# Optimization experiments

Measured on AMD Instinct MI355X. Metric: run time of the kernel, lower is better.

Reference implementation:

```python
import math
import jax, jax.numpy as jnp
import numpy as np

D_MODEL = 1024
NHEAD = 16
NUM_TEMP = 4
HEAD = D_MODEL // NHEAD          # 64
DIM = HEAD // NUM_TEMP           # 16
SCALE = math.sqrt(HEAD)
B, L = 2, 2048


def _make_freq():
    # freq = 10000^(-arange(0,dim,2)/dim), repeat_interleave(2) -> length DIM
    f = np.power(10000.0, -np.arange(0, DIM, 2) / DIM)
    return jnp.asarray(np.repeat(f, 2), dtype=jnp.float32)  # (DIM,)


def setup_inputs() -> dict:
    key = jax.random.key(0)
    ks = jax.random.split(key, 8)
    s = 0.02
    return {
        "data": jax.random.normal(ks[0], (B, L, D_MODEL), jnp.float32),
        "temporal": jax.random.uniform(ks[1], (B, L, NUM_TEMP), jnp.float32),
        "mask": jnp.zeros((L, L), jnp.float32),
        "Wq": jax.random.normal(ks[2], (D_MODEL, D_MODEL), jnp.float32) * s,
        "bq": jnp.zeros((D_MODEL,), jnp.float32),
        "Wk": jax.random.normal(ks[3], (D_MODEL, D_MODEL), jnp.float32) * s,
        "bk": jnp.zeros((D_MODEL,), jnp.float32),
        "Wv": jax.random.normal(ks[4], (D_MODEL, D_MODEL), jnp.float32) * s,
        "bv": jnp.zeros((D_MODEL,), jnp.float32),
    }


def _rotate_half_pairs(x):
    # [-x2, x1, -x4, x3, ...] along last dim
    stacked = jnp.stack([-x[..., 1::2], x[..., 0::2]], axis=-1)
    return stacked.reshape(x.shape)


def _apply_rotary(x, sine, cosine):
    # x: (B,L,H,HEAD); sine/cosine: (B,L,HEAD)
    return x * cosine[:, :, None, :] + _rotate_half_pairs(x) * sine[:, :, None, :]


def reference(data, temporal, mask, Wq, bq, Wk, bk, Wv, bv):
    freq = _make_freq()  # (DIM,)
    b, l, _ = data.shape
    q = (data @ Wq + bq).reshape(b, l, NHEAD, HEAD)
    k = (data @ Wk + bk).reshape(b, l, NHEAD, HEAD)
    v = (data @ Wv + bv).reshape(b, l, NHEAD, HEAD)
    # per-temporal-column frequencies: (B,L,T,DIM) -> (B,L,HEAD)
    freqs = (temporal[..., None] * freq).reshape(b, l, HEAD)
    cosine = jnp.cos(freqs)
    sine = jnp.sin(freqs)
    rq = _apply_rotary(q, sine, cosine)
    rk = _apply_rotary(k, sine, cosine)
    logits = jnp.einsum("bqhs,bkhs->bhqk", rq, rk) / SCALE + mask
    weights = jax.nn.softmax(logits, axis=-1)  # dropout is identity at eval
    context = jnp.einsum("bhqk,bkhs->bqhs", weights, v)
    return context.reshape(b, l, D_MODEL)
```

## Files before the change

kernel.cpp:

```cpp
#include <hip/hip_runtime.h>
#include <hip/hip_bf16.h>

#define LSEQ 2048
#define DM   1024
#define NH   16

typedef __attribute__((ext_vector_type(8)))  short bf16x8;
typedef __attribute__((ext_vector_type(8)))  unsigned short u16x8;
typedef __attribute__((ext_vector_type(4)))  float f32x4;
typedef __attribute__((ext_vector_type(16))) float f32x16;
typedef __attribute__((ext_vector_type(4)))  unsigned int u32x4;

#define LOG2E 1.4426950408889634f
#define C1SC  0.18033688011112042f

static __device__ __forceinline__ float exp2fast(float x) {
  return __builtin_amdgcn_exp2f(x);
}

static __device__ __forceinline__ unsigned short f2bf(float f) {
  unsigned int u = __float_as_uint(f);
  u += 0x7FFFu + ((u >> 16) & 1u);
  return (unsigned short)(u >> 16);
}

static __device__ __forceinline__ unsigned pk2(float a, float b) {
  __hip_bfloat162 t = __float22bfloat162_rn(make_float2(a, b));
  return *reinterpret_cast<unsigned*>(&t);
}

static __device__ __forceinline__ f32x16 unpack16(u16x8 a, u16x8 b) {
  const u32x4 ua = __builtin_bit_cast(u32x4, a);
  const u32x4 ub = __builtin_bit_cast(u32x4, b);
  f32x16 r;
#pragma unroll
  for (int i = 0; i < 4; ++i) {
    r[2 * i]     = __uint_as_float(ua[i] << 16);
    r[2 * i + 1] = __uint_as_float(ua[i] & 0xFFFF0000u);
    r[8 + 2 * i]     = __uint_as_float(ub[i] << 16);
    r[8 + 2 * i + 1] = __uint_as_float(ub[i] & 0xFFFF0000u);
  }
  return r;
}

static __device__ __forceinline__ bf16x8 pack8(float a, float b, float c, float d,
                                               float e, float f, float g, float h) {
  u32x4 w;
  w[0] = pk2(a, b); w[1] = pk2(c, d); w[2] = pk2(e, f); w[3] = pk2(g, h);
  return __builtin_bit_cast(bf16x8, w);
}

static __device__ __forceinline__ void gld_lds16(const unsigned short* g, unsigned short* l) {
  __builtin_amdgcn_global_load_lds(
      (const __attribute__((address_space(1))) unsigned int*)g,
      (__attribute__((address_space(3))) unsigned int*)l, 16, 0, 0);
}

__global__ void k_convert_data(const float* __restrict__ src,
                               unsigned short* __restrict__ dst, int n4) {
  int i = blockIdx.x * 256 + threadIdx.x;
  if (i >= n4) return;
  float4 v = reinterpret_cast<const float4*>(src)[i];
  ushort4 o;
  o.x = f2bf(v.x); o.y = f2bf(v.y); o.z = f2bf(v.z); o.w = f2bf(v.w);
  reinterpret_cast<ushort4*>(dst)[i] = o;
}

__global__ void k_transpose_w(const float* __restrict__ Wq,
                              const float* __restrict__ Wk,
                              const float* __restrict__ Wv,
                              unsigned short* __restrict__ Wt) {
  __shared__ unsigned short tile[64][65];
  const float* W = (blockIdx.z == 0) ? Wq : (blockIdx.z == 1) ? Wk : Wv;
  int n0 = blockIdx.x * 64, k0 = blockIdx.y * 64;
  int t = threadIdx.x;
  int c = t & 63, r0 = t >> 6;
  for (int i = 0; i < 16; ++i) {
    int r = r0 + i * 4;
    tile[r][c] = f2bf(W[(size_t)(k0 + r) * DM + n0 + c]);
  }
  __syncthreads();
  size_t nbase = (size_t)blockIdx.z * DM + n0;
  for (int i = 0; i < 16; ++i) {
    int n = r0 + i * 4;
    Wt[(nbase + n) * DM + k0 + c] = tile[c][n];
  }
}

__global__ void k_maskC(const float* __restrict__ mask,
                        unsigned short* __restrict__ maskCb,
                        int* __restrict__ zflags) {
  __shared__ float tile[64][65];
  __shared__ int nz;
  int q0 = blockIdx.x * 64, kv0 = blockIdx.y * 64;
  int t = threadIdx.x;
  if (t == 0) nz = 0;
  __syncthreads();
  int c = t & 63, r0 = t >> 6;
  int lnz = 0;
  for (int i = 0; i < 16; ++i) {
    int r = r0 + i * 4;
    float v = mask[(size_t)(q0 + r) * LSEQ + kv0 + c];
    tile[r][c] = v;
    lnz |= (v != 0.0f);
  }
  if (lnz) atomicOr(&nz, 1);
  __syncthreads();
  const int q = t & 63, slot = t >> 6;
  const int tt = slot >> 1, hh = slot & 1;
  u16x8 va, vb;
#pragma unroll
  for (int r = 0; r < 8; ++r) {
    const int kvloc = 32 * tt + 4 * hh + (r & 3) + 8 * (r >> 2);
    va[r] = f2bf(tile[q][kvloc] * LOG2E);
  }
#pragma unroll
  for (int r = 8; r < 16; ++r) {
    const int kvloc = 32 * tt + 4 * hh + (r & 3) + 8 * (r >> 2);
    vb[r - 8] = f2bf(tile[q][kvloc] * LOG2E);
  }
  unsigned short* dst = maskCb + ((size_t)((kv0 >> 6) * 4 + slot) * 2048 + q0 + q) * 16;
  *reinterpret_cast<u16x8*>(dst) = va;
  *reinterpret_cast<u16x8*>(dst + 8) = vb;
  if (t == 0) zflags[blockIdx.y * 32 + blockIdx.x] = (nz == 0);
}

__global__ __launch_bounds__(256) void k_qkv_gemm(
    const unsigned short* __restrict__ A, const unsigned short* __restrict__ Bt,
    const float* __restrict__ bq, const float* __restrict__ bk,
    const float* __restrict__ bv, const float* __restrict__ temporal,
    unsigned short* __restrict__ qbuf, unsigned short* __restrict__ kbuf,
    unsigned short* __restrict__ vtbuf) {
  __shared__ unsigned short As[128 * 32];
  __shared__ unsigned short Bs[128 * 32];
  __shared__ unsigned short otile[128 * 136];
  const int tid = threadIdx.x;
  const int lane = tid & 63, wid = tid >> 6;
  const int wm = wid >> 1, wn = wid & 1;
  const int lr = lane & 15, lg = lane >> 4;

  const int bid = blockIdx.x;
  const int xcd = bid & 7, rr = bid >> 3;
  const int mblk = xcd * 4 + (rr / 24);
  const int nblk = rr % 24;
  const int m0 = mblk * 128;
  const int n0 = nblk * 128;

  f32x4 acc[4][4] = {};

  const int e0 = tid * 8;
  const int e1 = (256 + tid) * 8;
  const int ra0 = e0 >> 5, ca0 = e0 & 31;
  const int ra1 = e1 >> 5, ca1 = e1 & 31;
  unsigned short* lA0 = As + wid * 512;
  unsigned short* lA1 = As + 2048 + wid * 512;
  unsigned short* lB0 = Bs + wid * 512;
  unsigned short* lB1 = Bs + 2048 + wid * 512;

  for (int k0 = 0; k0 < DM; k0 += 32) {
    __syncthreads();
    gld_lds16(A + (size_t)(m0 + ra0) * DM + k0 + ca0, lA0);
    gld_lds16(A + (size_t)(m0 + ra1) * DM + k0 + ca1, lA1);
    gld_lds16(Bt + (size_t)(n0 + ra0) * DM + k0 + ca0, lB0);
    gld_lds16(Bt + (size_t)(n0 + ra1) * DM + k0 + ca1, lB1);
    __syncthreads();
    bf16x8 af[4], bfv[4];
    for (int mi = 0; mi < 4; ++mi)
      af[mi] = *reinterpret_cast<const bf16x8*>(As + (wm * 64 + mi * 16 + lr) * 32 + lg * 8);
    for (int ni = 0; ni < 4; ++ni)
      bfv[ni] = *reinterpret_cast<const bf16x8*>(Bs + (wn * 64 + ni * 16 + lr) * 32 + lg * 8);
    for (int mi = 0; mi < 4; ++mi)
      for (int ni = 0; ni < 4; ++ni)
        acc[mi][ni] = __builtin_amdgcn_mfma_f32_16x16x32_bf16(af[mi], bfv[ni], acc[mi][ni], 0, 0, 0);
  }

  const int mat = n0 >> 10;
  const int c0 = n0 & 1023;
  const int bb = m0 >> 11;
  const int mloc = m0 & 2047;
  const float qscale = (mat == 0) ? C1SC : 1.f;

  for (int mi = 0; mi < 4; ++mi) {
    const int rrel_base = wm * 64 + mi * 16 + lg * 4;
    for (int ni = 0; ni < 4; ++ni) {
      const int crel = wn * 64 + ni * 16 + lr;
      const int c = (c0 + crel);
      const int d = c & 63;
      const float bias = (mat == 0 ? bq : mat == 1 ? bk : bv)[c];
      f32x4 v = acc[mi][ni];
      if (mat < 2) {
        const int jj = d & 15, tt = d >> 4;
        const float fr = __expf(-(float)(jj & 14) * 0.5756462732485115f);
        const float sign = (d & 1) ? 1.f : -1.f;
        for (int j = 0; j < 4; ++j) {
          const int rrel = rrel_base + j;
          const float x = v[j] + bias;
          const float part = __shfl_xor(x, 1, 64);
          const int lqs = mloc + rrel;
          const float fq = temporal[((size_t)bb * LSEQ + lqs) * 4 + tt] * fr;
          float sn, cs;
          __sincosf(fq, &sn, &cs);
          otile[rrel * 136 + crel] = f2bf((x * cs + sign * part * sn) * qscale);
        }
      } else {
        for (int j = 0; j < 4; ++j) {
          const int rrel = rrel_base + j;
          otile[crel * 136 + rrel] = f2bf(v[j] + bias);
        }
      }
    }
  }
  __syncthreads();

  for (int i = 0; i < 2; ++i) {
    const int h = (c0 >> 6) + i;
    const size_t bh = (size_t)(bb * NH + h);
    if (mat == 0) {
      const size_t base = (bh * LSEQ + mloc) * 64;
#pragma unroll
      for (int kk2 = 0; kk2 < 4; ++kk2) {
        const int e = kk2 * 2048 + tid * 8;
        const int r = e >> 6, d = e & 63;
        *reinterpret_cast<u16x8*>(qbuf + base + e) =
            *reinterpret_cast<const u16x8*>(otile + r * 136 + i * 64 + d);
      }
    } else if (mat == 1) {
      const size_t base = bh * 131072 + (size_t)(mloc >> 5) * 2048;
#pragma unroll
      for (int kk2 = 0; kk2 < 4; ++kk2) {
        const int e = kk2 * 2048 + tid * 8;
        const int r = kk2 * 32 + ((tid >> 1) & 31);
        const int d = ((tid >> 6) & 3) * 16 + (tid & 1) * 8;
        *reinterpret_cast<u16x8*>(kbuf + base + e) =
            *reinterpret_cast<const u16x8*>(otile + r * 136 + i * 64 + d);
      }
    } else {
      const size_t base = bh * 131072 + (size_t)(mloc >> 4) * 1024;
#pragma unroll
      for (int kk2 = 0; kk2 < 4; ++kk2) {
        const int e = kk2 * 2048 + tid * 8;
        const int d = ((tid >> 6) & 1) * 32 + ((tid >> 1) & 31);
        const int rb = (kk2 * 2 + (tid >> 7)) * 16;
        const int dl = (tid & 1) * 4;
        const unsigned short* srow = otile + (i * 64 + d) * 136 + rb + dl;
        ushort4 lo = *reinterpret_cast<const ushort4*>(srow);
        ushort4 hi4 = *reinterpret_cast<const ushort4*>(srow + 8);
        u16x8 w;
        w[0] = lo.x; w[1] = lo.y; w[2] = lo.z; w[3] = lo.w;
        w[4] = hi4.x; w[5] = hi4.y; w[6] = hi4.z; w[7] = hi4.w;
        *reinterpret_cast<u16x8*>(vtbuf + base + e) = w;
      }
    }
  }
}

__global__ __launch_bounds__(256) void k_attn(
    const unsigned short* __restrict__ qbuf, const unsigned short* __restrict__ kbuf,
    const unsigned short* __restrict__ vtbuf, const unsigned short* __restrict__ maskCb,
    const int* __restrict__ zflags, float* __restrict__ out) {
  __shared__ float otile[4][64][33];
  __shared__ float mlbuf[4][32][2];
  const int tid = threadIdx.x, lane = tid & 63, wid = tid >> 6;
  const int lq = lane & 31, hi = lane >> 5;
  const int qsub = wid & 1, kvh = wid >> 1;
  const int bh = blockIdx.y;
  const int q0 = blockIdx.x * 64 + qsub * 32;
  const int qg = q0 + lq;
  const size_t bhL = (size_t)bh * LSEQ;
  const unsigned short* kb = kbuf + (size_t)bh * 131072;
  const unsigned short* vb = vtbuf + (size_t)bh * 131072;
  const unsigned short* mb = maskCb + ((size_t)hi * 2048 + qg) * 16;

  bf16x8 qf[4];
#pragma unroll
  for (int c = 0; c < 4; ++c)
    qf[c] = *reinterpret_cast<const bf16x8*>(qbuf + (bhL + qg) * 64 + c * 16 + hi * 8);

  f32x16 o0 = {}, o1 = {};
  float m2 = 2.0f, l_run = 0.f;

  const int kv_beg = kvh * 1024, kv_end = kv_beg + 1024;
  for (int kv0 = kv_beg; kv0 < kv_end; kv0 += 64) {
    f32x16 s0, s1;
    const int zf = zflags[(kv0 >> 6) * 32 + blockIdx.x];
    if (zf) {
      s0 = (f32x16){};
      s1 = (f32x16){};
    } else {
      const unsigned short* mt = mb + (size_t)(kv0 >> 6) * (4 * 2048 * 16);
      s0 = unpack16(*reinterpret_cast<const u16x8*>(mt),
                    *reinterpret_cast<const u16x8*>(mt + 8));
      s1 = unpack16(*reinterpret_cast<const u16x8*>(mt + 2 * 2048 * 16),
                    *reinterpret_cast<const u16x8*>(mt + 2 * 2048 * 16 + 8));
    }

    const unsigned short* kch = kb + (size_t)(kv0 >> 5) * 2048;
#pragma unroll
    for (int c = 0; c < 4; ++c) {
      bf16x8 k0 = *reinterpret_cast<const bf16x8*>(kch + c * 512 + lq * 16 + hi * 8);
      bf16x8 k1 = *reinterpret_cast<const bf16x8*>(kch + 2048 + c * 512 + lq * 16 + hi * 8);
      s0 = __builtin_amdgcn_mfma_f32_32x32x16_bf16(k0, qf[c], s0, 0, 0, 0);
      s1 = __builtin_amdgcn_mfma_f32_32x32x16_bf16(k1, qf[c], s1, 0, 0, 0);
    }

    float rs0 = 0.f, rs1 = 0.f, rs2 = 0.f, rs3 = 0.f;
#pragma unroll
    for (int r = 0; r < 4; ++r) {
      s0[r] = exp2fast(s0[r] - m2);        rs0 += s0[r];
      s0[r + 4] = exp2fast(s0[r + 4] - m2);   rs1 += s0[r + 4];
      s0[r + 8] = exp2fast(s0[r + 8] - m2);   rs2 += s0[r + 8];
      s0[r + 12] = exp2fast(s0[r + 12] - m2); rs3 += s0[r + 12];
    }
#pragma unroll
    for (int r = 0; r < 4; ++r) {
      s1[r] = exp2fast(s1[r] - m2);        rs0 += s1[r];
      s1[r + 4] = exp2fast(s1[r + 4] - m2);   rs1 += s1[r + 4];
      s1[r + 8] = exp2fast(s1[r + 8] - m2);   rs2 += s1[r + 8];
      s1[r + 12] = exp2fast(s1[r + 12] - m2); rs3 += s1[r + 12];
    }
    float rs = (rs0 + rs1) + (rs2 + rs3);

    if (__any(rs > 2048.f)) {
      const float cc = 0.000244140625f;
#pragma unroll
      for (int r = 0; r < 16; ++r) { s0[r] *= cc; s1[r] *= cc; }
      rs *= cc; l_run *= cc;
#pragma unroll
      for (int r = 0; r < 16; ++r) { o0[r] *= cc; o1[r] *= cc; }
      m2 += 12.f;
    }

    rs += __shfl_xor(rs, 32, 64);
    l_run += rs;

    bf16x8 pf0 = pack8(s0[0], s0[1], s0[2], s0[3], s0[4], s0[5], s0[6], s0[7]);
    bf16x8 pf1 = pack8(s0[8], s0[9], s0[10], s0[11], s0[12], s0[13], s0[14], s0[15]);
    bf16x8 pf2 = pack8(s1[0], s1[1], s1[2], s1[3], s1[4], s1[5], s1[6], s1[7]);
    bf16x8 pf3 = pack8(s1[8], s1[9], s1[10], s1[11], s1[12], s1[13], s1[14], s1[15]);

    const unsigned short* vch = vb + (size_t)(kv0 >> 4) * 1024;
#pragma unroll
    for (int ks = 0; ks < 4; ++ks) {
      bf16x8 pf = (ks == 0) ? pf0 : (ks == 1) ? pf1 : (ks == 2) ? pf2 : pf3;
      bf16x8 v0 = *reinterpret_cast<const bf16x8*>(vch + ks * 1024 + lq * 16 + hi * 8);
      bf16x8 v1 = *reinterpret_cast<const bf16x8*>(vch + ks * 1024 + 512 + lq * 16 + hi * 8);
      o0 = __builtin_amdgcn_mfma_f32_32x32x16_bf16(v0, pf, o0, 0, 0, 0);
      o1 = __builtin_amdgcn_mfma_f32_32x32x16_bf16(v1, pf, o1, 0, 0, 0);
    }
  }

  if (lane < 32) { mlbuf[wid][lq][0] = m2; mlbuf[wid][lq][1] = l_run; }
  __syncthreads();
  const int pw = wid ^ 2;
  const float m_p = mlbuf[pw][lq][0];
  const float l_p = mlbuf[pw][lq][1];
  const float mstar = fmaxf(m2, m_p);
  const float f  = exp2fast(m2 - mstar);
  const float fp = exp2fast(m_p - mstar);
  const float scale = f / (l_run * f + l_p * fp);

#pragma unroll
  for (int r = 0; r < 16; ++r) {
    const int d = (r & 3) + 8 * (r >> 2) + 4 * hi;
    otile[wid][d][lq] = o0[r] * scale;
    otile[wid][32 + d][lq] = o1[r] * scale;
  }
  __syncthreads();

  const int b = bh >> 4, h = bh & 15;
#pragma unroll
  for (int i = 0; i < 4; ++i) {
    const int u = i * 256 + tid;
    const int q = u >> 4, c4 = u & 15;
    const int qs = q >> 5, ql = q & 31;
    float4 w;
    w.x = otile[qs][c4 * 4 + 0][ql] + otile[2 + qs][c4 * 4 + 0][ql];
    w.y = otile[qs][c4 * 4 + 1][ql] + otile[2 + qs][c4 * 4 + 1][ql];
    w.z = otile[qs][c4 * 4 + 2][ql] + otile[2 + qs][c4 * 4 + 2][ql];
    w.w = otile[qs][c4 * 4 + 3][ql] + otile[2 + qs][c4 * 4 + 3][ql];
    *reinterpret_cast<float4*>(
        out + ((size_t)(b * LSEQ + blockIdx.x * 64 + q)) * DM + h * 64 + c4 * 4) = w;
  }
}

extern "C" void kernel_launch(void* const* d_in, const int* in_sizes, int n_in,
                              void* d_out, int out_size, void* d_ws, size_t ws_size,
                              hipStream_t stream) {
  const float* data     = (const float*)d_in[0];
  const float* temporal = (const float*)d_in[1];
  const float* mask     = (const float*)d_in[2];
  const float* Wq       = (const float*)d_in[3];
  const float* bq       = (const float*)d_in[4];
  const float* Wk       = (const float*)d_in[5];
  const float* bk       = (const float*)d_in[6];
  const float* Wv       = (const float*)d_in[7];
  const float* bv       = (const float*)d_in[8];
  float* out = (float*)d_out;

  char* ws = (char*)d_ws;
  unsigned short* data_bf = (unsigned short*)(ws);
  unsigned short* wt      = (unsigned short*)(ws + (size_t)8  * 1048576);
  unsigned short* qbuf    = (unsigned short*)(ws + (size_t)14 * 1048576);
  unsigned short* kbuf    = (unsigned short*)(ws + (size_t)22 * 1048576);
  unsigned short* vtbuf   = (unsigned short*)(ws + (size_t)30 * 1048576);
  unsigned short* maskCb  = data_bf;
  int* zflags             = (int*)wt;

  hipLaunchKernelGGL(k_convert_data, dim3(4096), dim3(256), 0, stream,
                     data, data_bf, (2 * LSEQ * DM) / 4);
  hipLaunchKernelGGL(k_transpose_w, dim3(16, 16, 3), dim3(256), 0, stream,
                     Wq, Wk, Wv, wt);
  hipLaunchKernelGGL(k_qkv_gemm, dim3(768), dim3(256), 0, stream,
                     data_bf, wt, bq, bk, bv, temporal, qbuf, kbuf, vtbuf);
  hipLaunchKernelGGL(k_maskC, dim3(32, 32), dim3(256), 0, stream,
                     mask, maskCb, zflags);
  hipLaunchKernelGGL(k_attn, dim3(32, 32), dim3(256), 0, stream,
                     qbuf, kbuf, vtbuf, maskCb, zflags, out);
}
```

Measured before the change: 143.6 us.

## Process two 32-row query tiles per wave to reuse K/V fragments

Each wave now handles 64 queries as two 32-row sub-tiles, A and B, and applies every loaded K and V fragment to both. The grid along the query axis is halved and the output staging tile widened to match. This is meant to halve the global/L2 traffic for K, V and the zero flags per query, and to give the MFMA units more independent work. In exchange, register pressure roughly doubles, which may lower occupancy. With fewer blocks, the GPU may also be less well filled.

```diff
diff --git a/kernel.cpp b/kernel.cpp
--- a/kernel.cpp
+++ b/kernel.cpp
@@ -43,10 +43,10 @@
   return r;
 }
 
-static __device__ __forceinline__ bf16x8 pack8(float a, float b, float c, float d,
-                                               float e, float f, float g, float h) {
+static __device__ __forceinline__ bf16x8 pack8(const f32x16& s, int base) {
   u32x4 w;
-  w[0] = pk2(a, b); w[1] = pk2(c, d); w[2] = pk2(e, f); w[3] = pk2(g, h);
+  w[0] = pk2(s[base + 0], s[base + 1]); w[1] = pk2(s[base + 2], s[base + 3]);
+  w[2] = pk2(s[base + 4], s[base + 5]); w[3] = pk2(s[base + 6], s[base + 7]);
   return __builtin_bit_cast(bf16x8, w);
 }
 
@@ -258,40 +258,49 @@
     const unsigned short* __restrict__ qbuf, const unsigned short* __restrict__ kbuf,
     const unsigned short* __restrict__ vtbuf, const unsigned short* __restrict__ maskCb,
     const int* __restrict__ zflags, float* __restrict__ out) {
-  __shared__ float otile[4][64][33];
-  __shared__ float mlbuf[4][32][2];
+  __shared__ float otile[4][64][65];
+  __shared__ float mlbuf[4][2][32][2];
   const int tid = threadIdx.x, lane = tid & 63, wid = tid >> 6;
   const int lq = lane & 31, hi = lane >> 5;
-  const int qsub = wid & 1, kvh = wid >> 1;
+  const int qh = wid & 1, kvh = wid >> 1;
   const int bh = blockIdx.y;
-  const int q0 = blockIdx.x * 64 + qsub * 32;
-  const int qg = q0 + lq;
+  const int q0 = blockIdx.x * 128 + qh * 64;
+  const int qgA = q0 + lq, qgB = q0 + 32 + lq;
   const size_t bhL = (size_t)bh * LSEQ;
   const unsigned short* kb = kbuf + (size_t)bh * 131072;
   const unsigned short* vb = vtbuf + (size_t)bh * 131072;
-  const unsigned short* mb = maskCb + ((size_t)hi * 2048 + qg) * 16;
-
-  bf16x8 qf[4];
-#pragma unroll
-  for (int c = 0; c < 4; ++c)
-    qf[c] = *reinterpret_cast<const bf16x8*>(qbuf + (bhL + qg) * 64 + c * 16 + hi * 8);
-
-  f32x16 o0 = {}, o1 = {};
-  float m2 = 2.0f, l_run = 0.f;
+  const unsigned short* mbA = maskCb + ((size_t)hi * 2048 + qgA) * 16;
+  const unsigned short* mbB = maskCb + ((size_t)hi * 2048 + qgB) * 16;
+
+  bf16x8 qfA[4], qfB[4];
+#pragma unroll
+  for (int c = 0; c < 4; ++c) {
+    qfA[c] = *reinterpret_cast<const bf16x8*>(qbuf + (bhL + qgA) * 64 + c * 16 + hi * 8);
+    qfB[c] = *reinterpret_cast<const bf16x8*>(qbuf + (bhL + qgB) * 64 + c * 16 + hi * 8);
+  }
+
+  f32x16 oA0 = {}, oA1 = {}, oB0 = {}, oB1 = {};
+  float m2 = 2.0f, lA = 0.f, lB = 0.f;
 
   const int kv_beg = kvh * 1024, kv_end = kv_beg + 1024;
   for (int kv0 = kv_beg; kv0 < kv_end; kv0 += 64) {
-    f32x16 s0, s1;
-    const int zf = zflags[(kv0 >> 6) * 32 + blockIdx.x];
+    f32x16 sA0, sA1, sB0, sB1;
+    const int zf = zflags[(kv0 >> 6) * 32 + (q0 >> 6)];
     if (zf) {
-      s0 = (f32x16){};
-      s1 = (f32x16){};
+      sA0 = (f32x16){}; sA1 = (f32x16){};
+      sB0 = (f32x16){}; sB1 = (f32x16){};
     } else {
-      const unsigned short* mt = mb + (size_t)(kv0 >> 6) * (4 * 2048 * 16);
-      s0 = unpack16(*reinterpret_cast<const u16x8*>(mt),
-                    *reinterpret_cast<const u16x8*>(mt + 8));
-      s1 = unpack16(*reinterpret_cast<const u16x8*>(mt + 2 * 2048 * 16),
-                    *reinterpret_cast<const u16x8*>(mt + 2 * 2048 * 16 + 8));
+      const size_t mo = (size_t)(kv0 >> 6) * (4 * 2048 * 16);
+      const unsigned short* mtA = mbA + mo;
+      const unsigned short* mtB = mbB + mo;
+      sA0 = unpack16(*reinterpret_cast<const u16x8*>(mtA),
+                     *reinterpret_cast<const u16x8*>(mtA + 8));
+      sA1 = unpack16(*reinterpret_cast<const u16x8*>(mtA + 2 * 2048 * 16),
+                     *reinterpret_cast<const u16x8*>(mtA + 2 * 2048 * 16 + 8));
+      sB0 = unpack16(*reinterpret_cast<const u16x8*>(mtB),
+                     *reinterpret_cast<const u16x8*>(mtB + 8));
+      sB1 = unpack16(*reinterpret_cast<const u16x8*>(mtB + 2 * 2048 * 16),
+                     *reinterpret_cast<const u16x8*>(mtB + 2 * 2048 * 16 + 8));
     }
 
     const unsigned short* kch = kb + (size_t)(kv0 >> 5) * 2048;
@@ -299,87 +308,101 @@
     for (int c = 0; c < 4; ++c) {
       bf16x8 k0 = *reinterpret_cast<const bf16x8*>(kch + c * 512 + lq * 16 + hi * 8);
       bf16x8 k1 = *reinterpret_cast<const bf16x8*>(kch + 2048 + c * 512 + lq * 16 + hi * 8);
-      s0 = __builtin_amdgcn_mfma_f32_32x32x16_bf16(k0, qf[c], s0, 0, 0, 0);
-      s1 = __builtin_amdgcn_mfma_f32_32x32x16_bf16(k1, qf[c], s1, 0, 0, 0);
-    }
-
-    float rs0 = 0.f, rs1 = 0.f, rs2 = 0.f, rs3 = 0.f;
-#pragma unroll
-    for (int r = 0; r < 4; ++r) {
-      s0[r] = exp2fast(s0[r] - m2);        rs0 += s0[r];
-      s0[r + 4] = exp2fast(s0[r + 4] - m2);   rs1 += s0[r + 4];
-      s0[r + 8] = exp2fast(s0[r + 8] - m2);   rs2 += s0[r + 8];
-      s0[r + 12] = exp2fast(s0[r + 12] - m2); rs3 += s0[r + 12];
-    }
-#pragma unroll
-    for (int r = 0; r < 4; ++r) {
-      s1[r] = exp2fast(s1[r] - m2);        rs0 += s1[r];
-      s1[r + 4] = exp2fast(s1[r + 4] - m2);   rs1 += s1[r + 4];
-      s1[r + 8] = exp2fast(s1[r + 8] - m2);   rs2 += s1[r + 8];
-      s1[r + 12] = exp2fast(s1[r + 12] - m2); rs3 += s1[r + 12];
-    }
-    float rs = (rs0 + rs1) + (rs2 + rs3);
-
-    if (__any(rs > 2048.f)) {
+      sA0 = __builtin_amdgcn_mfma_f32_32x32x16_bf16(k0, qfA[c], sA0, 0, 0, 0);
+      sB0 = __builtin_amdgcn_mfma_f32_32x32x16_bf16(k0, qfB[c], sB0, 0, 0, 0);
+      sA1 = __builtin_amdgcn_mfma_f32_32x32x16_bf16(k1, qfA[c], sA1, 0, 0, 0);
+      sB1 = __builtin_amdgcn_mfma_f32_32x32x16_bf16(k1, qfB[c], sB1, 0, 0, 0);
+    }
+
+    float a0 = 0.f, a1 = 0.f, b0 = 0.f, b1 = 0.f;
+#pragma unroll
+    for (int r = 0; r < 8; ++r) {
+      sA0[r] = exp2fast(sA0[r] - m2);     a0 += sA0[r];
+      sA0[r + 8] = exp2fast(sA0[r + 8] - m2); a1 += sA0[r + 8];
+      sB0[r] = exp2fast(sB0[r] - m2);     b0 += sB0[r];
+      sB0[r + 8] = exp2fast(sB0[r + 8] - m2); b1 += sB0[r + 8];
+    }
+#pragma unroll
+    for (int r = 0; r < 8; ++r) {
+      sA1[r] = exp2fast(sA1[r] - m2);     a0 += sA1[r];
+      sA1[r + 8] = exp2fast(sA1[r + 8] - m2); a1 += sA1[r + 8];
+      sB1[r] = exp2fast(sB1[r] - m2);     b0 += sB1[r];
+      sB1[r + 8] = exp2fast(sB1[r + 8] - m2); b1 += sB1[r + 8];
+    }
+    float rsA = a0 + a1, rsB = b0 + b1;
+
+    if (__any(fmaxf(rsA, rsB) > 2048.f)) {
       const float cc = 0.000244140625f;
 #pragma unroll
-      for (int r = 0; r < 16; ++r) { s0[r] *= cc; s1[r] *= cc; }
-      rs *= cc; l_run *= cc;
-#pragma unroll
-      for (int r = 0; r < 16; ++r) { o0[r] *= cc; o1[r] *= cc; }
+      for (int r = 0; r < 16; ++r) {
+        sA0[r] *= cc; sA1[r] *= cc; sB0[r] *= cc; sB1[r] *= cc;
+        oA0[r] *= cc; oA1[r] *= cc; oB0[r] *= cc; oB1[r] *= cc;
+      }
+      rsA *= cc; rsB *= cc; lA *= cc; lB *= cc;
       m2 += 12.f;
     }
 
-    rs += __shfl_xor(rs, 32, 64);
-    l_run += rs;
-
-    bf16x8 pf0 = pack8(s0[0], s0[1], s0[2], s0[3], s0[4], s0[5], s0[6], s0[7]);
-    bf16x8 pf1 = pack8(s0[8], s0[9], s0[10], s0[11], s0[12], s0[13], s0[14], s0[15]);
-    bf16x8 pf2 = pack8(s1[0], s1[1], s1[2], s1[3], s1[4], s1[5], s1[6], s1[7]);
-    bf16x8 pf3 = pack8(s1[8], s1[9], s1[10], s1[11], s1[12], s1[13], s1[14], s1[15]);
+    rsA += __shfl_xor(rsA, 32, 64);
+    rsB += __shfl_xor(rsB, 32, 64);
+    lA += rsA; lB += rsB;
+
+    bf16x8 pfA0 = pack8(sA0, 0), pfA1 = pack8(sA0, 8);
+    bf16x8 pfA2 = pack8(sA1, 0), pfA3 = pack8(sA1, 8);
+    bf16x8 pfB0 = pack8(sB0, 0), pfB1 = pack8(sB0, 8);
+    bf16x8 pfB2 = pack8(sB1, 0), pfB3 = pack8(sB1, 8);
 
     const unsigned short* vch = vb + (size_t)(kv0 >> 4) * 1024;
 #pragma unroll
     for (int ks = 0; ks < 4; ++ks) {
-      bf16x8 pf = (ks == 0) ? pf0 : (ks == 1) ? pf1 : (ks == 2) ? pf2 : pf3;
+      bf16x8 pfA = (ks == 0) ? pfA0 : (ks == 1) ? pfA1 : (ks == 2) ? pfA2 : pfA3;
+      bf16x8 pfB = (ks == 0) ? pfB0 : (ks == 1) ? pfB1 : (ks == 2) ? pfB2 : pfB3;
       bf16x8 v0 = *reinterpret_cast<const bf16x8*>(vch + ks * 1024 + lq * 16 + hi * 8);
       bf16x8 v1 = *reinterpret_cast<const bf16x8*>(vch + ks * 1024 + 512 + lq * 16 + hi * 8);
-      o0 = __builtin_amdgcn_mfma_f32_32x32x16_bf16(v0, pf, o0, 0, 0, 0);
-      o1 = __builtin_amdgcn_mfma_f32_32x32x16_bf16(v1, pf, o1, 0, 0, 0);
-    }
-  }
-
-  if (lane < 32) { mlbuf[wid][lq][0] = m2; mlbuf[wid][lq][1] = l_run; }
+      oA0 = __builtin_amdgcn_mfma_f32_32x32x16_bf16(v0, pfA, oA0, 0, 0, 0);
+      oB0 = __builtin_amdgcn_mfma_f32_32x32x16_bf16(v0, pfB, oB0, 0, 0, 0);
+      oA1 = __builtin_amdgcn_mfma_f32_32x32x16_bf16(v1, pfA, oA1, 0, 0, 0);
+      oB1 = __builtin_amdgcn_mfma_f32_32x32x16_bf16(v1, pfB, oB1, 0, 0, 0);
+    }
+  }
+
+  if (lane < 32) {
+    mlbuf[wid][0][lq][0] = m2; mlbuf[wid][0][lq][1] = lA;
+    mlbuf[wid][1][lq][0] = m2; mlbuf[wid][1][lq][1] = lB;
+  }
   __syncthreads();
   const int pw = wid ^ 2;
-  const float m_p = mlbuf[pw][lq][0];
-  const float l_p = mlbuf[pw][lq][1];
-  const float mstar = fmaxf(m2, m_p);
-  const float f  = exp2fast(m2 - mstar);
-  const float fp = exp2fast(m_p - mstar);
-  const float scale = f / (l_run * f + l_p * fp);
+  const float mAp = mlbuf[pw][0][lq][0], lAp = mlbuf[pw][0][lq][1];
+  const float mBp = mlbuf[pw][1][lq][0], lBp = mlbuf[pw][1][lq][1];
+  const float msA = fmaxf(m2, mAp);
+  const float fA = exp2fast(m2 - msA), fAp = exp2fast(mAp - msA);
+  const float scaleA = fA / (lA * fA + lAp * fAp);
+  const float msB = fmaxf(m2, mBp);
+  const float fB = exp2fast(m2 - msB), fBp = exp2fast(mBp - msB);
+  const float scaleB = fB / (lB * fB + lBp * fBp);
 
 #pragma unroll
   for (int r = 0; r < 16; ++r) {
     const int d = (r & 3) + 8 * (r >> 2) + 4 * hi;
-    otile[wid][d][lq] = o0[r] * scale;
-    otile[wid][32 + d][lq] = o1[r] * scale;
+    otile[wid][d][lq] = oA0[r] * scaleA;
+    otile[wid][32 + d][lq] = oA1[r] * scaleA;
+    otile[wid][d][32 + lq] = oB0[r] * scaleB;
+    otile[wid][32 + d][32 + lq] = oB1[r] * scaleB;
   }
   __syncthreads();
 
   const int b = bh >> 4, h = bh & 15;
 #pragma unroll
-  for (int i = 0; i < 4; ++i) {
+  for (int i = 0; i < 8; ++i) {
     const int u = i * 256 + tid;
     const int q = u >> 4, c4 = u & 15;
-    const int qs = q >> 5, ql = q & 31;
+    const int qh2 = q >> 6, ql = q & 63;
     float4 w;
-    w.x = otile[qs][c4 * 4 + 0][ql] + otile[2 + qs][c4 * 4 + 0][ql];
-    w.y = otile[qs][c4 * 4 + 1][ql] + otile[2 + qs][c4 * 4 + 1][ql];
-    w.z = otile[qs][c4 * 4 + 2][ql] + otile[2 + qs][c4 * 4 + 2][ql];
-    w.w = otile[qs][c4 * 4 + 3][ql] + otile[2 + qs][c4 * 4 + 3][ql];
+    w.x = otile[qh2][c4 * 4 + 0][ql] + otile[2 + qh2][c4 * 4 + 0][ql];
+    w.y = otile[qh2][c4 * 4 + 1][ql] + otile[2 + qh2][c4 * 4 + 1][ql];
+    w.z = otile[qh2][c4 * 4 + 2][ql] + otile[2 + qh2][c4 * 4 + 2][ql];
+    w.w = otile[qh2][c4 * 4 + 3][ql] + otile[2 + qh2][c4 * 4 + 3][ql];
     *reinterpret_cast<float4*>(
-        out + ((size_t)(b * LSEQ + blockIdx.x * 64 + q)) * DM + h * 64 + c4 * 4) = w;
+        out + ((size_t)(b * LSEQ + blockIdx.x * 128 + q)) * DM + h * 64 + c4 * 4) = w;
   }
 }
 
@@ -414,6 +437,6 @@
                      data_bf, wt, bq, bk, bv, temporal, qbuf, kbuf, vtbuf);
   hipLaunchKernelGGL(k_maskC, dim3(32, 32), dim3(256), 0, stream,
                      mask, maskCb, zflags);
-  hipLaunchKernelGGL(k_attn, dim3(32, 32), dim3(256), 0, stream,
+  hipLaunchKernelGGL(k_attn, dim3(16, 32), dim3(256), 0, stream,
                      qbuf, kbuf, vtbuf, maskCb, zflags, out);
 }
```

Result: faster. 136.8 us (-4.7%).
